# Kernel optimization log

Measured on AMD Instinct MI355X. Metric: run time of the kernel, lower is better.

## Reference

```python
import jax, jax.numpy as jnp
import numpy as np

INF = 1.0e6  # 'infinity' for squared EDT; max real value is ~3*128^2 ~ 5e4


def edt_1d_sq(f, axis):
    """One pass of Felzenszwalb separable squared EDT along `axis`.
    d[i] = min_j f[j] + (i - j)^2  (brute-force vectorized lower envelope)."""
    f = jnp.moveaxis(f, axis, -1)
    n = f.shape[-1]
    i = jnp.arange(n, dtype=f.dtype)
    sq = (i[:, None] - i[None, :]) ** 2  # (n, n)
    d = jnp.min(f[..., None, :] + sq, axis=-1)  # (..., n)
    return jnp.moveaxis(d, -1, axis)


def compute_fg_dtm(mask):
    """Euclidean distance transform of foreground (distance to nearest background),
    matching scipy.ndimage.distance_transform_edt applied per batch element on the
    (C, X, Y, Z) mask (C==1 so the channel axis pass is the identity).
    mask: bool (B, 1, X, Y, Z) -> float32 (B, 1, X, Y, Z)."""
    def per_b(m):
        g = jnp.where(m, jnp.float32(INF), jnp.float32(0.0))
        for ax in range(m.ndim):
            g = edt_1d_sq(g, ax)
        return jnp.sqrt(g)
    return jax.lax.map(per_b, mask)


def setup_inputs() -> dict:
    key = jax.random.key(0)
    k1, k2, k3 = jax.random.split(key, 3)
    B, C, X, Y, Z = 2, 2, 128, 128, 128
    return {
        "outputs": jax.random.normal(k1, (B, C, X, Y, Z), dtype=jnp.float32),
        "outputs_dist": jax.random.normal(k2, (B, C, X, Y, Z), dtype=jnp.float32) * 10.0,
        "y": jax.random.randint(k3, (B, 1, X, Y, Z), 0, 2),
        "distance_map_weight": 1.0,
    }


def reference(outputs, outputs_dist, y, distance_map_weight):
    n_pred_ch = outputs.shape[1]
    # MONAI one_hot: (B,1,X,Y,Z) int labels -> (B,C,X,Y,Z) float
    y1h = jnp.moveaxis(jax.nn.one_hot(y[:, 0], n_pred_ch, dtype=outputs.dtype), -1, 1)
    x = outputs[:, 1:]            # foreground logits (B, 1, X, Y, Z)
    t = y1h[:, 1:]                # foreground mask
    od = outputs_dist[:, 1:]
    gt_dis = compute_fg_dtm(t > 0.5)
    # BCE with logits (mean reduction), numerically stable
    loss_ce = jnp.mean(jnp.maximum(x, 0.0) - x * t + jnp.log1p(jnp.exp(-jnp.abs(x))))
    # dice loss, flattened per batch element
    N = x.shape[0]
    smooth = jnp.float32(1.0)
    p = jax.nn.sigmoid(x).reshape(N, -1)
    tf = t.reshape(N, -1)
    dice = (2.0 * jnp.sum(p * tf, axis=1) + smooth) / (jnp.sum(p, axis=1) + jnp.sum(tf, axis=1) + smooth)
    loss_dice = 1.0 - jnp.sum(dice) / N
    # weighted L1 on the distance head, masked by the foreground mask
    msum = jnp.sum(t)
    loss_dist = jnp.where(
        msum == 0,
        jnp.float32(0.0),
        jnp.sum(jnp.abs(od - gt_dis) * t) / jnp.maximum(msum, jnp.float32(1e-12)),
    )
    return loss_ce + loss_dice + distance_map_weight * loss_dist
```

## Files before the change

kernel.cpp:

```cpp
#include <hip/hip_runtime.h>
#include <math.h>

#define M_SPATIAL 2097152
#define MV4 (M_SPATIAL / 4)

__device__ __forceinline__ float wave_redf(float v) {
#pragma unroll
  for (int o = 32; o > 0; o >>= 1) v += __shfl_down(v, o, 64);
  return v;
}
__device__ __forceinline__ double wave_redd(double v) {
#pragma unroll
  for (int o = 32; o > 0; o >>= 1) v += __shfl_down(v, o, 64);
  return v;
}


__global__ __launch_bounds__(256) void kA_ce(const float4* __restrict__ outputs4,
                                             const int4* __restrict__ y4,
                                             double* __restrict__ part) {
  int blk = blockIdx.x;
  int base = blk * 1024;
  int b = (blk >= 512) ? 1 : 0;
  const float4* xc = outputs4 + (size_t)(b * 2 + 1) * MV4;
  float ce = 0.f, ps = 0.f, pts = 0.f, tsum = 0.f;
#pragma unroll
  for (int k = 0; k < 4; ++k) {
    int v4 = base + (int)threadIdx.x + k * 256;
    int s4 = v4 & (MV4 - 1);
    int4 yv = y4[v4];
    float4 x = xc[s4];
#define ELEM(c, yc)                                                         \
    {                                                                       \
      float t = (yc == 1) ? 1.0f : 0.0f;                                    \
      float xx = x.c;                                                       \
      ce += fmaxf(xx, 0.0f) - xx * t + log1pf(expf(-fabsf(xx)));            \
      float p = 1.0f / (1.0f + expf(-xx));                                  \
      ps += p; pts += p * t; tsum += t;                                     \
    }
    ELEM(x, yv.x) ELEM(y, yv.y) ELEM(z, yv.z) ELEM(w, yv.w)
#undef ELEM
  }
  float r0 = wave_redf(ce), r1 = wave_redf(ps), r2 = wave_redf(pts), r3 = wave_redf(tsum);
  __shared__ float sm[4][4];
  int lane = threadIdx.x & 63, w = threadIdx.x >> 6;
  if (lane == 0) { sm[w][0] = r0; sm[w][1] = r1; sm[w][2] = r2; sm[w][3] = r3; }
  __syncthreads();
  if (threadIdx.x == 0) {
    part[blk]        = (double)(sm[0][0] + sm[1][0] + sm[2][0] + sm[3][0]);
    part[1024 + blk] = (double)(sm[0][1] + sm[1][1] + sm[2][1] + sm[3][1]);
    part[2048 + blk] = (double)(sm[0][2] + sm[1][2] + sm[2][2] + sm[3][2]);
    part[3072 + blk] = (double)(sm[0][3] + sm[1][3] + sm[2][3] + sm[3][3]);
  }
}

__global__ __launch_bounds__(64) void kB_edtx(const int* __restrict__ y,
                                              float* __restrict__ g) {
  __shared__ int df[128 * 64];
  int blk = blockIdx.x;
  int b  = blk >> 8;
  int yy = (blk >> 1) & 127;
  int zc = blk & 1;
  int l  = threadIdx.x;
  size_t base = (size_t)b * M_SPATIAL + (size_t)yy * 128 + (size_t)zc * 64 + l;

  int d = 200;
  for (int u0 = 0; u0 < 128; u0 += 16) {
    int yb[16];
#pragma unroll
    for (int k = 0; k < 16; ++k) yb[k] = y[base + (size_t)(u0 + k) * 16384];
#pragma unroll
    for (int k = 0; k < 16; ++k) {
      int fg = (yb[k] == 1);
      d = fg ? ((d < 200) ? d + 1 : 200) : 0;
      df[(u0 + k) * 64 + l] = d;
    }
  }
  float hinf = 1000000.f + (float)(yy * yy);
  float yy2f = (float)(yy * yy);
  int db = 200;
  for (int u0 = 127; u0 >= 0; u0 -= 16) {
    int fv[16];
#pragma unroll
    for (int k = 0; k < 16; ++k) fv[k] = df[(u0 - k) * 64 + l];
    float ov[16];
#pragma unroll
    for (int k = 0; k < 16; ++k) {
      db = (fv[k] > 0) ? ((db < 200) ? db + 1 : 200) : 0;
      int m = min(fv[k], db);
      ov[k] = (m >= 128) ? hinf : ((float)(m * m) + yy2f);
    }
#pragma unroll
    for (int k = 0; k < 16; ++k) g[base + (size_t)(u0 - k) * 16384] = ov[k];
  }
}

__global__ __launch_bounds__(256) void kC_edty(float* __restrict__ g) {
  __shared__ float hl[128 * 33];
  int blk = blockIdx.x;
  int b = blk >> 9, xx = (blk >> 2) & 127, zc = blk & 3;
  int t = threadIdx.x;
  size_t rb = (size_t)b * M_SPATIAL + (size_t)xx * 16384 + (size_t)zc * 32;

#pragma unroll
  for (int r = 0; r < 4; ++r) {
    int i4 = t + r * 256;
    int j = i4 >> 3, w = i4 & 7;
    float4 v = *(const float4*)(g + rb + (size_t)j * 128 + 4 * w);
    hl[j * 33 + 4 * w + 0] = v.x;
    hl[j * 33 + 4 * w + 1] = v.y;
    hl[j * 33 + 4 * w + 2] = v.z;
    hl[j * 33 + 4 * w + 3] = v.w;
  }
  __syncthreads();

  int zl = t & 31, ig = t >> 5;
  float best[16], mc[16];
#pragma unroll
  for (int k = 0; k < 16; ++k) {
    best[k] = 3.0e38f;
    mc[k] = -2.0f * (float)(ig * 16 + k);
  }
#pragma unroll 4
  for (int j = 0; j < 128; ++j) {
    float hj = hl[j * 33 + zl];
    float jf = (float)j;
#pragma unroll
    for (int k = 0; k < 16; ++k) best[k] = fminf(best[k], fmaf(mc[k], jf, hj));
  }
  int gz = zc * 32 + zl;
  float zq = (float)(gz * gz);
  size_t ob = rb + zl;
#pragma unroll
  for (int k = 0; k < 16; ++k) {
    int i = ig * 16 + k;
    float dY = (float)(i * i) + best[k];
    g[ob + (size_t)i * 128] = dY + zq;
  }
}

__global__ __launch_bounds__(256) void kD_edtz_dist(const float* __restrict__ g,
                                                    const float* __restrict__ od,
                                                    double* __restrict__ part) {
  __shared__ float hl[128 * 33];
  __shared__ float sred[4];
  int blk = blockIdx.x;
  int b = blk >> 9, xx = (blk >> 2) & 127, yc = blk & 3;
  int t = threadIdx.x;
  size_t rb = (size_t)b * M_SPATIAL + (size_t)xx * 16384 + (size_t)yc * 4096;
  int yl = t & 31, ig = t >> 5;

  size_t odb = (size_t)(2 * b + 1) * M_SPATIAL + (size_t)xx * 16384 +
               (size_t)yc * 4096 + (size_t)yl * 128 + (size_t)ig * 16;
  const float4* o4 = (const float4*)(od + odb);
  float4 ov[4];
#pragma unroll
  for (int r = 0; r < 4; ++r) ov[r] = o4[r];

  const float4* h4 = (const float4*)(g + rb);
#pragma unroll
  for (int r = 0; r < 4; ++r) {
    int i4 = t + r * 256;
    float4 v = h4[i4];
    int flat = i4 * 4;
    int z = flat & 127, yw = flat >> 7;
    hl[(z + 0) * 33 + yw] = v.x;
    hl[(z + 1) * 33 + yw] = v.y;
    hl[(z + 2) * 33 + yw] = v.z;
    hl[(z + 3) * 33 + yw] = v.w;
  }
  __syncthreads();

  float best[16], mc[16];
#pragma unroll
  for (int k = 0; k < 16; ++k) {
    best[k] = 3.0e38f;
    mc[k] = -2.0f * (float)(ig * 16 + k);
  }
#pragma unroll 4
  for (int j = 0; j < 128; ++j) {
    float hj = hl[j * 33 + yl];
    float jf = (float)j;
#pragma unroll
    for (int k = 0; k < 16; ++k) best[k] = fminf(best[k], fmaf(mc[k], jf, hj));
  }
  const float* of = (const float*)ov;
  float dist = 0.f;
#pragma unroll
  for (int k = 0; k < 16; ++k) {
    int i = ig * 16 + k;
    float dv = (float)(i * i) + best[k];
    if (dv > 0.f) dist += fabsf(of[k] - sqrtf(dv));
  }
  float r = wave_redf(dist);
  int lane = t & 63, w = t >> 6;
  if (lane == 0) sred[w] = r;
  __syncthreads();
  if (t == 0) part[4096 + blk] = (double)(sred[0] + sred[1] + sred[2] + sred[3]);
}

__global__ __launch_bounds__(256) void k_final(const double* __restrict__ part,
                                               const float* __restrict__ wptr,
                                               float* __restrict__ out) {
  int i = threadIdx.x;
  double ce  = part[i] + part[i + 256] + part[i + 512] + part[i + 768];
  double p0  = part[1024 + i] + part[1024 + i + 256];
  double p1  = part[1536 + i] + part[1536 + i + 256];
  double pt0 = part[2048 + i] + part[2048 + i + 256];
  double pt1 = part[2560 + i] + part[2560 + i + 256];
  double t0  = part[3072 + i] + part[3072 + i + 256];
  double t1  = part[3584 + i] + part[3584 + i + 256];
  double ds  = part[4096 + i] + part[4096 + i + 256] + part[4096 + i + 512] + part[4096 + i + 768];

  ce = wave_redd(ce); p0 = wave_redd(p0); p1 = wave_redd(p1);
  pt0 = wave_redd(pt0); pt1 = wave_redd(pt1);
  t0 = wave_redd(t0); t1 = wave_redd(t1); ds = wave_redd(ds);

  __shared__ double sm[4][8];
  int lane = threadIdx.x & 63, w = threadIdx.x >> 6;
  if (lane == 0) {
    sm[w][0] = ce; sm[w][1] = p0; sm[w][2] = p1; sm[w][3] = pt0;
    sm[w][4] = pt1; sm[w][5] = t0; sm[w][6] = t1; sm[w][7] = ds;
  }
  __syncthreads();
  if (threadIdx.x == 0) {
    double a[8];
    for (int q = 0; q < 8; ++q) a[q] = sm[0][q] + sm[1][q] + sm[2][q] + sm[3][q];
    double cem = a[0] / 4194304.0;
    double dice0 = (2.0 * a[3] + 1.0) / (a[1] + a[5] + 1.0);
    double dice1 = (2.0 * a[4] + 1.0) / (a[2] + a[6] + 1.0);
    double ldice = 1.0 - 0.5 * (dice0 + dice1);
    double msum = a[5] + a[6];
    double ldist = (msum == 0.0) ? 0.0 : a[7] / fmax(msum, 1e-12);
    out[0] = (float)(cem + ldice + (double)wptr[0] * ldist);
  }
}

extern "C" void kernel_launch(void* const* d_in, const int* in_sizes, int n_in,
                              void* d_out, int out_size, void* d_ws, size_t ws_size,
                              hipStream_t stream) {
  const float* outputs      = (const float*)d_in[0];
  const float* outputs_dist = (const float*)d_in[1];
  const int*   y            = (const int*)d_in[2];
  const float* wptr         = (const float*)d_in[3];
  float* out = (float*)d_out;

  double* part = (double*)d_ws;
  float* g = (float*)((char*)d_ws + 65536);

  kA_ce<<<1024, 256, 0, stream>>>((const float4*)outputs, (const int4*)y, part);
  kB_edtx<<<512, 64, 0, stream>>>(y, g);
  kC_edty<<<1024, 256, 0, stream>>>(g);
  kD_edtz_dist<<<1024, 256, 0, stream>>>(g, outputs_dist, part);
  k_final<<<1, 256, 0, stream>>>(part, wptr, out);
}
```

Measured before the change: 172.8 us.

## Parallelize x-pass EDT across chunks with shared-memory carries; pair-min in y/z passes

The x-direction distance pass used to run a sequential forward and backward scan of 128 elements per thread with 64-thread blocks and a large shared buffer. It now splits each column into 8 chunks of 16 handled by separate threads. Each thread finds its chunk's last and next background positions, and the neighbouring chunks' values are combined through shared memory to give the carries. This raises parallelism and occupancy and removes the 32KB LDS buffer, at the cost of a barrier and some redundant per-chunk work. Separately, the y and z brute-force min loops now process two j values per iteration with a nested fminf, to shorten the dependency chain on best[k].

```diff
diff --git a/kernel.cpp b/kernel.cpp
--- a/kernel.cpp
+++ b/kernel.cpp
@@ -54,45 +54,61 @@
   }
 }
 
-__global__ __launch_bounds__(64) void kB_edtx(const int* __restrict__ y,
-                                              float* __restrict__ g) {
-  __shared__ int df[128 * 64];
-  int blk = blockIdx.x;
-  int b  = blk >> 8;
-  int yy = (blk >> 1) & 127;
-  int zc = blk & 1;
-  int l  = threadIdx.x;
-  size_t base = (size_t)b * M_SPATIAL + (size_t)yy * 128 + (size_t)zc * 64 + l;
-
-  int d = 200;
-  for (int u0 = 0; u0 < 128; u0 += 16) {
-    int yb[16];
-#pragma unroll
-    for (int k = 0; k < 16; ++k) yb[k] = y[base + (size_t)(u0 + k) * 16384];
-#pragma unroll
-    for (int k = 0; k < 16; ++k) {
-      int fg = (yb[k] == 1);
-      d = fg ? ((d < 200) ? d + 1 : 200) : 0;
-      df[(u0 + k) * 64 + l] = d;
-    }
-  }
-  float hinf = 1000000.f + (float)(yy * yy);
+__global__ __launch_bounds__(256) void kB_edtx(const int* __restrict__ y,
+                                               float* __restrict__ g) {
+  int blk = blockIdx.x;
+  int b  = blk >> 9;
+  int yy = (blk >> 2) & 127;
+  int zq = blk & 3;
+  int t  = threadIdx.x;
+  int c  = t >> 5;
+  int zl = t & 31;
+  int x0 = c * 16;
+  size_t base = (size_t)b * M_SPATIAL + (size_t)yy * 128 + (size_t)zq * 32 + zl;
+
+  int yb[16];
+#pragma unroll
+  for (int k = 0; k < 16; ++k) yb[k] = y[base + (size_t)(x0 + k) * 16384];
+
+  int lastE = -200, nextE = 400;
+#pragma unroll
+  for (int k = 0; k < 16; ++k) lastE = (yb[k] == 1) ? lastE : (x0 + k);
+#pragma unroll
+  for (int k = 15; k >= 0; --k) nextE = (yb[k] == 1) ? nextE : (x0 + k);
+
+  __shared__ int lE[8][32];
+  __shared__ int nE[8][32];
+  lE[c][zl] = lastE;
+  nE[c][zl] = nextE;
+  __syncthreads();
+
+  int carryL = -200, carryN = 400;
+#pragma unroll
+  for (int q = 0; q < 7; ++q) {
+    if (q < c)     carryL = max(carryL, lE[q][zl]);
+    if (q + 1 > c) carryN = min(carryN, nE[q + 1][zl]);
+  }
+
   float yy2f = (float)(yy * yy);
-  int db = 200;
-  for (int u0 = 127; u0 >= 0; u0 -= 16) {
-    int fv[16];
-#pragma unroll
-    for (int k = 0; k < 16; ++k) fv[k] = df[(u0 - k) * 64 + l];
-    float ov[16];
-#pragma unroll
-    for (int k = 0; k < 16; ++k) {
-      db = (fv[k] > 0) ? ((db < 200) ? db + 1 : 200) : 0;
-      int m = min(fv[k], db);
-      ov[k] = (m >= 128) ? hinf : ((float)(m * m) + yy2f);
-    }
-#pragma unroll
-    for (int k = 0; k < 16; ++k) g[base + (size_t)(u0 - k) * 16384] = ov[k];
-  }
+  float hinf = 1000000.f + yy2f;
+
+  int df[16];
+  int ll = carryL;
+#pragma unroll
+  for (int k = 0; k < 16; ++k) {
+    ll = (yb[k] == 1) ? ll : (x0 + k);
+    df[k] = min(x0 + k - ll, 200);
+  }
+  float ov[16];
+  int nn = carryN;
+#pragma unroll
+  for (int k = 15; k >= 0; --k) {
+    nn = (yb[k] == 1) ? nn : (x0 + k);
+    int m = min(df[k], min(nn - (x0 + k), 200));
+    ov[k] = (m >= 128) ? hinf : ((float)(m * m) + yy2f);
+  }
+#pragma unroll
+  for (int k = 0; k < 16; ++k) g[base + (size_t)(x0 + k) * 16384] = ov[k];
 }
 
 __global__ __launch_bounds__(256) void kC_edty(float* __restrict__ g) {
@@ -121,12 +137,14 @@
     best[k] = 3.0e38f;
     mc[k] = -2.0f * (float)(ig * 16 + k);
   }
-#pragma unroll 4
-  for (int j = 0; j < 128; ++j) {
-    float hj = hl[j * 33 + zl];
-    float jf = (float)j;
-#pragma unroll
-    for (int k = 0; k < 16; ++k) best[k] = fminf(best[k], fmaf(mc[k], jf, hj));
+#pragma unroll 2
+  for (int j = 0; j < 128; j += 2) {
+    float h0 = hl[j * 33 + zl];
+    float h1 = hl[(j + 1) * 33 + zl];
+    float j0 = (float)j, j1 = (float)(j + 1);
+#pragma unroll
+    for (int k = 0; k < 16; ++k)
+      best[k] = fminf(fminf(fmaf(mc[k], j0, h0), fmaf(mc[k], j1, h1)), best[k]);
   }
   int gz = zc * 32 + zl;
   float zq = (float)(gz * gz);
@@ -177,12 +195,14 @@
     best[k] = 3.0e38f;
     mc[k] = -2.0f * (float)(ig * 16 + k);
   }
-#pragma unroll 4
-  for (int j = 0; j < 128; ++j) {
-    float hj = hl[j * 33 + yl];
-    float jf = (float)j;
-#pragma unroll
-    for (int k = 0; k < 16; ++k) best[k] = fminf(best[k], fmaf(mc[k], jf, hj));
+#pragma unroll 2
+  for (int j = 0; j < 128; j += 2) {
+    float h0 = hl[j * 33 + yl];
+    float h1 = hl[(j + 1) * 33 + yl];
+    float j0 = (float)j, j1 = (float)(j + 1);
+#pragma unroll
+    for (int k = 0; k < 16; ++k)
+      best[k] = fminf(fminf(fmaf(mc[k], j0, h0), fmaf(mc[k], j1, h1)), best[k]);
   }
   const float* of = (const float*)ov;
   float dist = 0.f;
@@ -249,7 +269,7 @@
   float* g = (float*)((char*)d_ws + 65536);
 
   kA_ce<<<1024, 256, 0, stream>>>((const float4*)outputs, (const int4*)y, part);
-  kB_edtx<<<512, 64, 0, stream>>>(y, g);
+  kB_edtx<<<1024, 256, 0, stream>>>(y, g);
   kC_edty<<<1024, 256, 0, stream>>>(g);
   kD_edtz_dist<<<1024, 256, 0, stream>>>(g, outputs_dist, part);
   k_final<<<1, 256, 0, stream>>>(part, wptr, out);
```

Result: faster. 166.8 us (-3.5%).
